# Kernel optimization log

Measured on AMD Instinct MI355X. Metric: run time of the kernel, lower is better.

Reference implementation:

```python
import jax, jax.numpy as jnp
import numpy as np


def conv2d_same(x, w, b=None):
    # x: [B,C,H,W], w: [O,I,kh,kw], stride 1, SAME padding (pad=1 for 3x3)
    out = jax.lax.conv_general_dilated(
        x, w, window_strides=(1, 1), padding='SAME',
        dimension_numbers=('NCHW', 'OIHW', 'NCHW'))
    if b is not None:
        out = out + b[None, :, None, None]
    return out


def deform_conv(x, offset, wd, k=3, pad=1, dg=4):
    # DCNv1: per-location offset-guided bilinear sampling + weighted accumulation.
    # x: [B,C,H,W]; offset: [B, dg*k*k*2, H, W] as (dy,dx) pairs per kernel tap;
    # wd: [O, C, k, k] (bias-free, as in mmcv DeformConv).
    B, C, H, W = x.shape
    cg = C // dg          # channels per deformable group
    K = k * k
    off = offset.reshape(B, dg, K, 2, H, W)
    dy, dx = off[:, :, :, 0], off[:, :, :, 1]          # [B,dg,K,H,W]
    ky = (jnp.arange(K) // k - pad).astype(x.dtype)    # kernel row offsets
    kx = (jnp.arange(K) % k - pad).astype(x.dtype)     # kernel col offsets
    hh = jnp.arange(H, dtype=x.dtype)
    ww = jnp.arange(W, dtype=x.dtype)
    py = dy + ky[None, None, :, None, None] + hh[None, None, None, :, None]
    px = dx + kx[None, None, :, None, None] + ww[None, None, None, None, :]
    y0 = jnp.floor(py); x0 = jnp.floor(px)
    wy1 = py - y0; wy0 = 1.0 - wy1
    wx1 = px - x0; wx0 = 1.0 - wx1
    xg = x.reshape(B, dg, cg, H * W)

    def gather(yi, xi):
        # zero outside the feature map (implicit zero padding of bilinear kernel)
        valid = (yi >= 0) & (yi < H) & (xi >= 0) & (xi < W)
        yc = jnp.clip(yi, 0, H - 1).astype(jnp.int32)
        xc = jnp.clip(xi, 0, W - 1).astype(jnp.int32)
        idx = (yc * W + xc).reshape(B, dg, 1, K * H * W)
        g = jnp.take_along_axis(xg, jnp.broadcast_to(idx, (B, dg, cg, K * H * W)), axis=-1)
        g = g.reshape(B, dg, cg, K, H, W)
        return g * valid[:, :, None].astype(x.dtype)

    val = (gather(y0, x0) * (wy0 * wx0)[:, :, None]
           + gather(y0, x0 + 1) * (wy0 * wx1)[:, :, None]
           + gather(y0 + 1, x0) * (wy1 * wx0)[:, :, None]
           + gather(y0 + 1, x0 + 1) * (wy1 * wx1)[:, :, None])  # [B,dg,cg,K,H,W]
    wr = wd.reshape(wd.shape[0], dg, cg, K)
    return jnp.einsum('ogck,bgckhw->bohw', wr, val)


def setup_inputs() -> dict:
    key = jax.random.key(0)
    k1, k2, k3, k4 = jax.random.split(key, 4)
    B, C, H, W = 8, 256, 64, 64
    dg, ks = 4, 3
    x = jax.random.normal(k1, (B, C, H, W), dtype=jnp.float32)
    w1 = jax.random.normal(k2, (C, C, 3, 3), dtype=jnp.float32) * 0.01
    b1 = jnp.zeros((C,), dtype=jnp.float32)
    w2 = jax.random.normal(k3, (dg * ks * ks * 2, C, 3, 3), dtype=jnp.float32) * 0.01
    b2 = jnp.zeros((dg * ks * ks * 2,), dtype=jnp.float32)
    wd = jax.random.normal(k4, (C, C, ks, ks), dtype=jnp.float32) * 0.01
    return {'x': x, 'w1': w1, 'b1': b1, 'w2': w2, 'b2': b2, 'wd': wd}


def reference(x, w1, b1, w2, b2, wd):
    # offset branch uses x.detach() in the original
    xd = jax.lax.stop_gradient(x)
    offset = conv2d_same(conv2d_same(xd, w1, b1), w2, b2)
    return jax.nn.relu(deform_conv(x, offset, wd, k=3, pad=1, dg=4))
```

## Files before the change

kernel.cpp:

```cpp
#include <hip/hip_runtime.h>
#include <hip/hip_bf16.h>


typedef __attribute__((ext_vector_type(8))) short bf16x8;
typedef __attribute__((ext_vector_type(4))) float f32x4;

static __device__ __forceinline__ ushort f2bf(float f) {
  __hip_bfloat16 h = __float2bfloat16(f);
  return *reinterpret_cast<ushort*>(&h);
}
static __device__ __forceinline__ float bf2f(ushort u) {
  union { uint u32; float f; } cv;
  cv.u32 = ((uint)u) << 16;
  return cv.f;
}

__global__ __launch_bounds__(256) void prep_weights(
    const float* __restrict__ w1, const float* __restrict__ w2,
    const float* __restrict__ wd,
    ushort* __restrict__ wt1s, ushort* __restrict__ wt2s,
    ushort* __restrict__ wtds) {
  const int N1 = 36 * 256 * 64;
  const int N2 = 36 * 80 * 64;
  const int N3 = 36 * 256 * 64;
  int total = N1 + N2 + N3;
  for (int i = blockIdx.x * 256 + threadIdx.x; i < total; i += gridDim.x * 256) {
    if (i < N1) {
      int e = i & 7, p = (i >> 3) & 7, co = (i >> 6) & 255, ti = i >> 14;
      int cc = ((p ^ (co & 7)) << 3) + e;
      int kk = ti >> 2, chunk = ti & 3;
      wt1s[i] = f2bf(w1[(co * 256 + chunk * 64 + cc) * 9 + kk]);
    } else if (i < N1 + N2) {
      int d = i - N1;
      int e = d & 7, p = (d >> 3) & 7;
      int r = d >> 6;
      int co = r % 80, ti = r / 80;
      int cc = ((p ^ (co & 7)) << 3) + e;
      int kk = ti >> 2, chunk = ti & 3;
      wt2s[d] = (co < 72) ? f2bf(w2[(co * 256 + chunk * 64 + cc) * 9 + kk])
                          : (ushort)0;
    } else {
      int d = i - N1 - N2;
      int e = d & 7, p = (d >> 3) & 7, co = (d >> 6) & 255, ti = d >> 14;
      int c = ((p ^ (co & 7)) << 3) + e;
      int g = ti / 9, kk = ti - g * 9;
      wtds[d] = f2bf(wd[(co * 256 + g * 64 + c) * 9 + kk]);
    }
  }
}

__global__ __launch_bounds__(256) void transpose_x(
    const float* __restrict__ x, ushort* __restrict__ xt) {
  int id = blockIdx.x;
  int y = id & 63, bg = id >> 6;
  int c = threadIdx.x & 63, xi = threadIdx.x >> 6;
  const float* ip = x + (((size_t)bg) << 18) + ((size_t)c << 12) + y * 64;
  ushort* op = xt + (((size_t)bg) << 18) + (size_t)y * 4096 + c;
#pragma unroll
  for (int j = 0; j < 16; ++j) {
    int xx = xi * 16 + j;
    op[(size_t)xx * 64] = f2bf(ip[xx]);
  }
}

template <int MODE, int MFR, int NFR, bool RELU, bool HASBIAS, bool OUT_CHLAST>
__global__ __launch_bounds__(128, 1) void fa_mfma4(
    const ushort* __restrict__ inT,
    const float* __restrict__ off,
    const char* __restrict__ wBs,
    const float* __restrict__ bias,
    void* __restrict__ outp,
    int co_total, int co_write) {
  constexpr int CO_TILE = NFR * 16;
  constexpr int TILE_B = CO_TILE * 128;
  constexpr int NCALLS = TILE_B / (128 * 16);
  constexpr int NRN = (MODE == 1) ? 8 : 2;
  __shared__ __align__(16) ushort Blds[2][CO_TILE * 64];

  int id = blockIdx.x;
  int id2 = (id & 7) * 64 + (id >> 3);
  int b = id2 >> 6, h = id2 & 63;
  int t = threadIdx.x;
  int wv = t >> 6, lane = t & 63;
  int ml = lane & 15, kc = lane >> 4;
  int ml7 = ml & 7;

  auto stage = [&](int ti, int bufsel) {
    const char* src0 = wBs + (size_t)ti * TILE_B + t * 16;
    ushort* dst0 = &Blds[bufsel][t * 8];
#pragma unroll
    for (int m = 0; m < NCALLS; ++m) {
      __builtin_amdgcn_global_load_lds(
          (const __attribute__((address_space(1))) void*)(src0 + m * 2048),
          (__attribute__((address_space(3))) void*)(dst0 + m * 1024), 16, 0, 0);
    }
  };

  int pcol[MFR];
#pragma unroll
  for (int mf = 0; mf < MFR; ++mf) pcol[mf] = wv * (MFR * 16) + mf * 16 + ml;

  const bf16x8 bz = {0, 0, 0, 0, 0, 0, 0, 0};
  bf16x8 aCur[MFR][2];
  bf16x8 rN[MFR][NRN];
  float wsv[MFR][4];
  float2 offA[MFR];

  auto issueA0 = [&](int tn) {
    int kk = tn >> 2, chunk = tn & 3;
    int ky = kk / 3, kx = kk - ky * 3;
    int gy = h + ky - 1;
    bool rowok = (gy >= 0) & (gy < 64);
#pragma unroll
    for (int mf = 0; mf < MFR; ++mf) {
      int gx = pcol[mf] + kx - 1;
      bool inb = rowok & (gx >= 0) & (gx < 64);
      const ushort* p =
          inT + ((((size_t)(b * 4 + chunk) << 12) + gy * 64 + gx) << 6) + kc * 8;
      rN[mf][0] = bz;
      rN[mf][1] = bz;
      if (inb) {
        rN[mf][0] = *(const bf16x8*)p;
        rN[mf][1] = *(const bf16x8*)(p + 32);
      }
    }
  };
  auto finishA0 = [&]() {
#pragma unroll
    for (int mf = 0; mf < MFR; ++mf) {
      aCur[mf][0] = rN[mf][0];
      aCur[mf][1] = rN[mf][1];
    }
  };

  auto loadOff = [&](int tn) {
    int g = tn / 9, kk = tn - 9 * (tn / 9);
    int ch = g * 18 + kk * 2;
#pragma unroll
    for (int mf = 0; mf < MFR; ++mf) {
      const float* offp =
          off + (((size_t)b * 72 + ch) << 12) + h * 64 + pcol[mf];
      offA[mf].x = offp[0];
      offA[mf].y = offp[4096];
    }
  };
  auto issueA1 = [&](int tn) {
    int g = tn / 9, kk = tn - 9 * (tn / 9);
    int ky = kk / 3, kx = kk - ky * 3;
    const ushort* base = inT + (((size_t)(b * 4 + g)) << 18) + kc * 8;
#pragma unroll
    for (int mf = 0; mf < MFR; ++mf) {
      float py = (float)(h + ky - 1) + offA[mf].x;
      float pxf = (float)(pcol[mf] + kx - 1) + offA[mf].y;
      float y0f = floorf(py), x0f = floorf(pxf);
      float wy1 = py - y0f, wx1 = pxf - x0f;
      float wy0 = 1.f - wy1, wx0 = 1.f - wx1;
      int y0 = (int)y0f, x0i = (int)x0f;
      int y1 = y0 + 1, x1i = x0i + 1;
      bool vy0 = (y0 >= 0) & (y0 < 64);
      bool vy1 = (y1 >= 0) & (y1 < 64);
      bool vx0 = (x0i >= 0) & (x0i < 64);
      bool vx1 = (x1i >= 0) & (x1i < 64);
      wsv[mf][0] = (vy0 & vx0) ? wy0 * wx0 : 0.f;
      wsv[mf][1] = (vy0 & vx1) ? wy0 * wx1 : 0.f;
      wsv[mf][2] = (vy1 & vx0) ? wy1 * wx0 : 0.f;
      wsv[mf][3] = (vy1 & vx1) ? wy1 * wx1 : 0.f;
      int yc0 = min(max(y0, 0), 63), yc1 = min(max(y1, 0), 63);
      int xc0 = min(max(x0i, 0), 63), xc1 = min(max(x1i, 0), 63);
      const ushort* p00 = base + ((yc0 * 64 + xc0) << 6);
      const ushort* p01 = base + ((yc0 * 64 + xc1) << 6);
      const ushort* p10 = base + ((yc1 * 64 + xc0) << 6);
      const ushort* p11 = base + ((yc1 * 64 + xc1) << 6);
      rN[mf][0] = *(const bf16x8*)p00;
      rN[mf][1] = *(const bf16x8*)(p00 + 32);
      rN[mf][2] = *(const bf16x8*)p01;
      rN[mf][3] = *(const bf16x8*)(p01 + 32);
      rN[mf][4] = *(const bf16x8*)p10;
      rN[mf][5] = *(const bf16x8*)(p10 + 32);
      rN[mf][6] = *(const bf16x8*)p11;
      rN[mf][7] = *(const bf16x8*)(p11 + 32);
    }
  };
  auto finishA1 = [&]() {
#pragma unroll
    for (int mf = 0; mf < MFR; ++mf) {
      float w00 = wsv[mf][0], w01 = wsv[mf][1];
      float w10 = wsv[mf][2], w11 = wsv[mf][3];
#pragma unroll
      for (int ks = 0; ks < 2; ++ks) {
        bf16x8 q00 = rN[mf][0 + ks], q01 = rN[mf][2 + ks];
        bf16x8 q10 = rN[mf][4 + ks], q11 = rN[mf][6 + ks];
        bf16x8 av;
#pragma unroll
        for (int jj = 0; jj < 4; ++jj) {
          float v0 = w00 * bf2f((ushort)q00[2 * jj]) + w01 * bf2f((ushort)q01[2 * jj]) +
                     w10 * bf2f((ushort)q10[2 * jj]) + w11 * bf2f((ushort)q11[2 * jj]);
          float v1 = w00 * bf2f((ushort)q00[2 * jj + 1]) + w01 * bf2f((ushort)q01[2 * jj + 1]) +
                     w10 * bf2f((ushort)q10[2 * jj + 1]) + w11 * bf2f((ushort)q11[2 * jj + 1]);
          av[2 * jj] = (short)f2bf(v0);
          av[2 * jj + 1] = (short)f2bf(v1);
        }
        aCur[mf][ks] = av;
      }
    }
  };

  f32x4 acc[MFR][NFR];
#pragma unroll
  for (int i = 0; i < MFR; ++i)
#pragma unroll
    for (int j = 0; j < NFR; ++j) acc[i][j] = (f32x4){0.f, 0.f, 0.f, 0.f};

  if (MODE == 1) {
    loadOff(0);
    issueA1(0);
    loadOff(1);
    finishA1();
  } else {
    issueA0(0);
    finishA0();
  }
  stage(0, 0);
  __syncthreads();

  for (int ti = 0; ti < 36; ++ti) {
    int cur = ti & 1;
    if (ti < 35) {
      stage(ti + 1, cur ^ 1);
      if (MODE == 1) issueA1(ti + 1); else issueA0(ti + 1);
    }
    if (MODE == 1 && ti < 34) loadOff(ti + 2);

#pragma unroll
    for (int ks = 0; ks < 2; ++ks) {
      int sw = (((ks * 4 + kc) ^ ml7) << 3);
      bf16x8 bq[NFR];
#pragma unroll
      for (int nf = 0; nf < NFR; ++nf)
        bq[nf] = *(const bf16x8*)&Blds[cur][(nf * 16 + ml) * 64 + sw];
#pragma unroll
      for (int mf = 0; mf < MFR; ++mf)
#pragma unroll
        for (int nf = 0; nf < NFR; ++nf)
          acc[mf][nf] = __builtin_amdgcn_mfma_f32_16x16x32_bf16(
              aCur[mf][ks], bq[nf], acc[mf][nf], 0, 0, 0);
    }

    if (ti < 35) { if (MODE == 1) finishA1(); else finishA0(); }
    __syncthreads();
  }

  int rq = lane >> 4;
#pragma unroll
  for (int nf = 0; nf < NFR; ++nf) {
    int cog = nf * 16 + ml;
    if (cog < co_write) {
      float bv = HASBIAS ? bias[cog] : 0.f;
#pragma unroll
      for (int mf = 0; mf < MFR; ++mf) {
#pragma unroll
        for (int ri = 0; ri < 4; ++ri) {
          int pxe = wv * (MFR * 16) + mf * 16 + rq * 4 + ri;
          float v = acc[mf][nf][ri] + bv;
          if (RELU) v = fmaxf(v, 0.f);
          if (OUT_CHLAST) {
            int g_out = cog >> 6, ci = cog & 63;
            ((ushort*)outp)[((((size_t)(b * 4 + g_out) << 12) + h * 64 + pxe) << 6) + ci] =
                f2bf(v);
          } else {
            ((float*)outp)[(((size_t)b * co_total + cog) << 12) + h * 64 + pxe] = v;
          }
        }
      }
    }
  }
}

extern "C" void kernel_launch(void* const* d_in, const int* in_sizes, int n_in,
                              void* d_out, int out_size, void* d_ws, size_t ws_size,
                              hipStream_t stream) {
  const float* x  = (const float*)d_in[0];
  const float* w1 = (const float*)d_in[1];
  const float* b1 = (const float*)d_in[2];
  const float* w2 = (const float*)d_in[3];
  const float* b2 = (const float*)d_in[4];
  const float* wd = (const float*)d_in[5];

  char* wsb = (char*)d_ws;
  float*  off_buf = (float*)wsb;
  ushort* xt      = (ushort*)(wsb + 9437184);
  ushort* wt1s    = (ushort*)(wsb + 26214400);
  ushort* wt2s    = (ushort*)(wsb + 27394048);
  ushort* wtds    = (ushort*)(wsb + 27762688);

  prep_weights<<<2048, 256, 0, stream>>>(w1, w2, wd, wt1s, wt2s, wtds);
  transpose_x<<<2048, 256, 0, stream>>>(x, xt);

  fa_mfma4<0, 2, 16, false, true, true>
      <<<512, 128, 0, stream>>>(xt, nullptr, (const char*)wt1s, b1, d_out, 256, 256);

  fa_mfma4<0, 2, 5, false, true, false>
      <<<512, 128, 0, stream>>>((const ushort*)d_out, nullptr, (const char*)wt2s,
                                b2, off_buf, 72, 72);

  fa_mfma4<1, 2, 16, true, false, false>
      <<<512, 128, 0, stream>>>(xt, off_buf, (const char*)wtds, nullptr, d_out,
                                256, 256);
}
```

Before: 204.3 us.

## Load weight fragments directly from global memory instead of LDS staging

Removes the double-buffered LDS staging of weight tiles (global_load_lds plus per-iteration __syncthreads) and has each lane read its B fragments straight from global memory, relying on L2/L1 caching. The weight prep no longer applies the XOR swizzle, since the swizzle was only there to avoid LDS bank conflicts. This drops the barriers and LDS traffic, at the cost of more per-wave global load latency and redundant reads of the same weights by both waves.

```diff
diff --git a/kernel.cpp b/kernel.cpp
--- a/kernel.cpp
+++ b/kernel.cpp
@@ -18,33 +18,29 @@
 __global__ __launch_bounds__(256) void prep_weights(
     const float* __restrict__ w1, const float* __restrict__ w2,
     const float* __restrict__ wd,
-    ushort* __restrict__ wt1s, ushort* __restrict__ wt2s,
-    ushort* __restrict__ wtds) {
+    ushort* __restrict__ wt1t, ushort* __restrict__ wt2t,
+    ushort* __restrict__ wtdt) {
   const int N1 = 36 * 256 * 64;
   const int N2 = 36 * 80 * 64;
   const int N3 = 36 * 256 * 64;
   int total = N1 + N2 + N3;
   for (int i = blockIdx.x * 256 + threadIdx.x; i < total; i += gridDim.x * 256) {
     if (i < N1) {
-      int e = i & 7, p = (i >> 3) & 7, co = (i >> 6) & 255, ti = i >> 14;
-      int cc = ((p ^ (co & 7)) << 3) + e;
+      int k6 = i & 63, co = (i >> 6) & 255, ti = i >> 14;
       int kk = ti >> 2, chunk = ti & 3;
-      wt1s[i] = f2bf(w1[(co * 256 + chunk * 64 + cc) * 9 + kk]);
+      wt1t[i] = f2bf(w1[(co * 256 + chunk * 64 + k6) * 9 + kk]);
     } else if (i < N1 + N2) {
       int d = i - N1;
-      int e = d & 7, p = (d >> 3) & 7;
-      int r = d >> 6;
+      int k6 = d & 63, r = d >> 6;
       int co = r % 80, ti = r / 80;
-      int cc = ((p ^ (co & 7)) << 3) + e;
       int kk = ti >> 2, chunk = ti & 3;
-      wt2s[d] = (co < 72) ? f2bf(w2[(co * 256 + chunk * 64 + cc) * 9 + kk])
+      wt2t[d] = (co < 72) ? f2bf(w2[(co * 256 + chunk * 64 + k6) * 9 + kk])
                           : (ushort)0;
     } else {
       int d = i - N1 - N2;
-      int e = d & 7, p = (d >> 3) & 7, co = (d >> 6) & 255, ti = d >> 14;
-      int c = ((p ^ (co & 7)) << 3) + e;
+      int k6 = d & 63, co = (d >> 6) & 255, ti = d >> 14;
       int g = ti / 9, kk = ti - g * 9;
-      wtds[d] = f2bf(wd[(co * 256 + g * 64 + c) * 9 + kk]);
+      wtdt[d] = f2bf(wd[(co * 256 + g * 64 + k6) * 9 + kk]);
     }
   }
 }
@@ -63,19 +59,17 @@
   }
 }
 
-template <int MODE, int MFR, int NFR, bool RELU, bool HASBIAS, bool OUT_CHLAST>
-__global__ __launch_bounds__(128, 1) void fa_mfma4(
+template <int MODE, int NFR, bool RELU, bool HASBIAS, bool OUT_CHLAST>
+__global__ __launch_bounds__(128, 1) void fa_mfma5(
     const ushort* __restrict__ inT,
     const float* __restrict__ off,
-    const char* __restrict__ wBs,
+    const ushort* __restrict__ wB,
     const float* __restrict__ bias,
     void* __restrict__ outp,
     int co_total, int co_write) {
+  constexpr int MFR = 2;
   constexpr int CO_TILE = NFR * 16;
-  constexpr int TILE_B = CO_TILE * 128;
-  constexpr int NCALLS = TILE_B / (128 * 16);
   constexpr int NRN = (MODE == 1) ? 8 : 2;
-  __shared__ __align__(16) ushort Blds[2][CO_TILE * 64];
 
   int id = blockIdx.x;
   int id2 = (id & 7) * 64 + (id >> 3);
@@ -83,18 +77,6 @@
   int t = threadIdx.x;
   int wv = t >> 6, lane = t & 63;
   int ml = lane & 15, kc = lane >> 4;
-  int ml7 = ml & 7;
-
-  auto stage = [&](int ti, int bufsel) {
-    const char* src0 = wBs + (size_t)ti * TILE_B + t * 16;
-    ushort* dst0 = &Blds[bufsel][t * 8];
-#pragma unroll
-    for (int m = 0; m < NCALLS; ++m) {
-      __builtin_amdgcn_global_load_lds(
-          (const __attribute__((address_space(1))) void*)(src0 + m * 2048),
-          (__attribute__((address_space(3))) void*)(dst0 + m * 1024), 16, 0, 0);
-    }
-  };
 
   int pcol[MFR];
 #pragma unroll
@@ -105,6 +87,8 @@
   bf16x8 rN[MFR][NRN];
   float wsv[MFR][4];
   float2 offA[MFR];
+
+  const ushort* wBl = wB + (ml << 6) + kc * 8;
 
   auto issueA0 = [&](int tn) {
     int kk = tn >> 2, chunk = tn & 3;
@@ -220,34 +204,41 @@
     issueA0(0);
     finishA0();
   }
-  stage(0, 0);
-  __syncthreads();
 
   for (int ti = 0; ti < 36; ++ti) {
-    int cur = ti & 1;
     if (ti < 35) {
-      stage(ti + 1, cur ^ 1);
       if (MODE == 1) issueA1(ti + 1); else issueA0(ti + 1);
     }
     if (MODE == 1 && ti < 34) loadOff(ti + 2);
 
-#pragma unroll
-    for (int ks = 0; ks < 2; ++ks) {
-      int sw = (((ks * 4 + kc) ^ ml7) << 3);
+    const ushort* wt = wBl + ((size_t)ti * CO_TILE << 6);
+
+    {
       bf16x8 bq[NFR];
 #pragma unroll
       for (int nf = 0; nf < NFR; ++nf)
-        bq[nf] = *(const bf16x8*)&Blds[cur][(nf * 16 + ml) * 64 + sw];
+        bq[nf] = *(const bf16x8*)(wt + (nf << 10));
 #pragma unroll
       for (int mf = 0; mf < MFR; ++mf)
 #pragma unroll
         for (int nf = 0; nf < NFR; ++nf)
           acc[mf][nf] = __builtin_amdgcn_mfma_f32_16x16x32_bf16(
-              aCur[mf][ks], bq[nf], acc[mf][nf], 0, 0, 0);
+              aCur[mf][0], bq[nf], acc[mf][nf], 0, 0, 0);
+    }
+    {
+      bf16x8 bq[NFR];
+#pragma unroll
+      for (int nf = 0; nf < NFR; ++nf)
+        bq[nf] = *(const bf16x8*)(wt + (nf << 10) + 32);
+#pragma unroll
+      for (int mf = 0; mf < MFR; ++mf)
+#pragma unroll
+        for (int nf = 0; nf < NFR; ++nf)
+          acc[mf][nf] = __builtin_amdgcn_mfma_f32_16x16x32_bf16(
+              aCur[mf][1], bq[nf], acc[mf][nf], 0, 0, 0);
     }
 
     if (ti < 35) { if (MODE == 1) finishA1(); else finishA0(); }
-    __syncthreads();
   }
 
   int rq = lane >> 4;
@@ -289,21 +280,20 @@
   char* wsb = (char*)d_ws;
   float*  off_buf = (float*)wsb;
   ushort* xt      = (ushort*)(wsb + 9437184);
-  ushort* wt1s    = (ushort*)(wsb + 26214400);
-  ushort* wt2s    = (ushort*)(wsb + 27394048);
-  ushort* wtds    = (ushort*)(wsb + 27762688);
-
-  prep_weights<<<2048, 256, 0, stream>>>(w1, w2, wd, wt1s, wt2s, wtds);
+  ushort* wt1t    = (ushort*)(wsb + 26214400);
+  ushort* wt2t    = (ushort*)(wsb + 27394048);
+  ushort* wtdt    = (ushort*)(wsb + 27762688);
+
+  prep_weights<<<2048, 256, 0, stream>>>(w1, w2, wd, wt1t, wt2t, wtdt);
   transpose_x<<<2048, 256, 0, stream>>>(x, xt);
 
-  fa_mfma4<0, 2, 16, false, true, true>
-      <<<512, 128, 0, stream>>>(xt, nullptr, (const char*)wt1s, b1, d_out, 256, 256);
-
-  fa_mfma4<0, 2, 5, false, true, false>
-      <<<512, 128, 0, stream>>>((const ushort*)d_out, nullptr, (const char*)wt2s,
-                                b2, off_buf, 72, 72);
-
-  fa_mfma4<1, 2, 16, true, false, false>
-      <<<512, 128, 0, stream>>>(xt, off_buf, (const char*)wtds, nullptr, d_out,
-                                256, 256);
-}
+  fa_mfma5<0, 16, false, true, true>
+      <<<512, 128, 0, stream>>>(xt, nullptr, wt1t, b1, d_out, 256, 256);
+
+  fa_mfma5<0, 5, false, true, false>
+      <<<512, 128, 0, stream>>>((const ushort*)d_out, nullptr, wt2t, b2,
+                                off_buf, 72, 72);
+
+  fa_mfma5<1, 16, true, false, false>
+      <<<512, 128, 0, stream>>>(xt, off_buf, wtdt, nullptr, d_out, 256, 256);
+}
```

Result: slower. 416.8 us (+104.0%).

## Split each row tile across four waves with one M-fragment each

Applied to the files above, without the earlier changes.

The conv/deform-conv MFMA kernel now launches 256 threads (4 waves) per row-block instead of 128 (2 waves). Each wave handles 16 pixels with a single M fragment rather than 32 pixels with two. Launch bounds allow 2 blocks per CU, and the weight staging is rewritten so 256 threads cover the tile with clamped addresses. The intent is to cut per-thread registers and raise occupancy and latency hiding for the gather-heavy deformable path. The cost is that each B-fragment LDS read now feeds half as many MFMAs, and the clamped staging re-reads some bytes.

```diff
diff --git a/kernel.cpp b/kernel.cpp
--- a/kernel.cpp
+++ b/kernel.cpp
@@ -63,8 +63,8 @@
   }
 }
 
-template <int MODE, int MFR, int NFR, bool RELU, bool HASBIAS, bool OUT_CHLAST>
-__global__ __launch_bounds__(128, 1) void fa_mfma4(
+template <int MODE, int NFR, bool RELU, bool HASBIAS, bool OUT_CHLAST>
+__global__ __launch_bounds__(256, 2) void fa_mfma6(
     const ushort* __restrict__ inT,
     const float* __restrict__ off,
     const char* __restrict__ wBs,
@@ -73,9 +73,9 @@
     int co_total, int co_write) {
   constexpr int CO_TILE = NFR * 16;
   constexpr int TILE_B = CO_TILE * 128;
-  constexpr int NCALLS = TILE_B / (128 * 16);
+  constexpr int NCALLS = (TILE_B + 4095) / 4096;
   constexpr int NRN = (MODE == 1) ? 8 : 2;
-  __shared__ __align__(16) ushort Blds[2][CO_TILE * 64];
+  __shared__ __align__(16) ushort Blds[2][NCALLS * 2048];
 
   int id = blockIdx.x;
   int id2 = (id & 7) * 64 + (id >> 3);
@@ -86,130 +86,109 @@
   int ml7 = ml & 7;
 
   auto stage = [&](int ti, int bufsel) {
-    const char* src0 = wBs + (size_t)ti * TILE_B + t * 16;
-    ushort* dst0 = &Blds[bufsel][t * 8];
 #pragma unroll
     for (int m = 0; m < NCALLS; ++m) {
+      int d = (m * 256 + t) * 16;
+      int ds = (d > TILE_B - 16) ? (TILE_B - 16) : d;
+      const char* src = wBs + (size_t)ti * TILE_B + ds;
+      ushort* dst = &Blds[bufsel][(m * 256 + t) * 8];
       __builtin_amdgcn_global_load_lds(
-          (const __attribute__((address_space(1))) void*)(src0 + m * 2048),
-          (__attribute__((address_space(3))) void*)(dst0 + m * 1024), 16, 0, 0);
-    }
-  };
-
-  int pcol[MFR];
-#pragma unroll
-  for (int mf = 0; mf < MFR; ++mf) pcol[mf] = wv * (MFR * 16) + mf * 16 + ml;
+          (const __attribute__((address_space(1))) void*)src,
+          (__attribute__((address_space(3))) void*)dst, 16, 0, 0);
+    }
+  };
+
+  const int pcol = wv * 16 + ml;
 
   const bf16x8 bz = {0, 0, 0, 0, 0, 0, 0, 0};
-  bf16x8 aCur[MFR][2];
-  bf16x8 rN[MFR][NRN];
-  float wsv[MFR][4];
-  float2 offA[MFR];
+  bf16x8 aCur[2];
+  bf16x8 rN[NRN];
+  float wsv[4];
+  float2 offA;
 
   auto issueA0 = [&](int tn) {
     int kk = tn >> 2, chunk = tn & 3;
     int ky = kk / 3, kx = kk - ky * 3;
-    int gy = h + ky - 1;
-    bool rowok = (gy >= 0) & (gy < 64);
-#pragma unroll
-    for (int mf = 0; mf < MFR; ++mf) {
-      int gx = pcol[mf] + kx - 1;
-      bool inb = rowok & (gx >= 0) & (gx < 64);
-      const ushort* p =
-          inT + ((((size_t)(b * 4 + chunk) << 12) + gy * 64 + gx) << 6) + kc * 8;
-      rN[mf][0] = bz;
-      rN[mf][1] = bz;
-      if (inb) {
-        rN[mf][0] = *(const bf16x8*)p;
-        rN[mf][1] = *(const bf16x8*)(p + 32);
-      }
+    int gy = h + ky - 1, gx = pcol + kx - 1;
+    bool inb = (gy >= 0) & (gy < 64) & (gx >= 0) & (gx < 64);
+    const ushort* p =
+        inT + ((((size_t)(b * 4 + chunk) << 12) + gy * 64 + gx) << 6) + kc * 8;
+    rN[0] = bz;
+    rN[1] = bz;
+    if (inb) {
+      rN[0] = *(const bf16x8*)p;
+      rN[1] = *(const bf16x8*)(p + 32);
     }
   };
   auto finishA0 = [&]() {
-#pragma unroll
-    for (int mf = 0; mf < MFR; ++mf) {
-      aCur[mf][0] = rN[mf][0];
-      aCur[mf][1] = rN[mf][1];
-    }
+    aCur[0] = rN[0];
+    aCur[1] = rN[1];
   };
 
   auto loadOff = [&](int tn) {
     int g = tn / 9, kk = tn - 9 * (tn / 9);
     int ch = g * 18 + kk * 2;
-#pragma unroll
-    for (int mf = 0; mf < MFR; ++mf) {
-      const float* offp =
-          off + (((size_t)b * 72 + ch) << 12) + h * 64 + pcol[mf];
-      offA[mf].x = offp[0];
-      offA[mf].y = offp[4096];
-    }
+    const float* offp = off + (((size_t)b * 72 + ch) << 12) + h * 64 + pcol;
+    offA.x = offp[0];
+    offA.y = offp[4096];
   };
   auto issueA1 = [&](int tn) {
     int g = tn / 9, kk = tn - 9 * (tn / 9);
     int ky = kk / 3, kx = kk - ky * 3;
     const ushort* base = inT + (((size_t)(b * 4 + g)) << 18) + kc * 8;
-#pragma unroll
-    for (int mf = 0; mf < MFR; ++mf) {
-      float py = (float)(h + ky - 1) + offA[mf].x;
-      float pxf = (float)(pcol[mf] + kx - 1) + offA[mf].y;
-      float y0f = floorf(py), x0f = floorf(pxf);
-      float wy1 = py - y0f, wx1 = pxf - x0f;
-      float wy0 = 1.f - wy1, wx0 = 1.f - wx1;
-      int y0 = (int)y0f, x0i = (int)x0f;
-      int y1 = y0 + 1, x1i = x0i + 1;
-      bool vy0 = (y0 >= 0) & (y0 < 64);
-      bool vy1 = (y1 >= 0) & (y1 < 64);
-      bool vx0 = (x0i >= 0) & (x0i < 64);
-      bool vx1 = (x1i >= 0) & (x1i < 64);
-      wsv[mf][0] = (vy0 & vx0) ? wy0 * wx0 : 0.f;
-      wsv[mf][1] = (vy0 & vx1) ? wy0 * wx1 : 0.f;
-      wsv[mf][2] = (vy1 & vx0) ? wy1 * wx0 : 0.f;
-      wsv[mf][3] = (vy1 & vx1) ? wy1 * wx1 : 0.f;
-      int yc0 = min(max(y0, 0), 63), yc1 = min(max(y1, 0), 63);
-      int xc0 = min(max(x0i, 0), 63), xc1 = min(max(x1i, 0), 63);
-      const ushort* p00 = base + ((yc0 * 64 + xc0) << 6);
-      const ushort* p01 = base + ((yc0 * 64 + xc1) << 6);
-      const ushort* p10 = base + ((yc1 * 64 + xc0) << 6);
-      const ushort* p11 = base + ((yc1 * 64 + xc1) << 6);
-      rN[mf][0] = *(const bf16x8*)p00;
-      rN[mf][1] = *(const bf16x8*)(p00 + 32);
-      rN[mf][2] = *(const bf16x8*)p01;
-      rN[mf][3] = *(const bf16x8*)(p01 + 32);
-      rN[mf][4] = *(const bf16x8*)p10;
-      rN[mf][5] = *(const bf16x8*)(p10 + 32);
-      rN[mf][6] = *(const bf16x8*)p11;
-      rN[mf][7] = *(const bf16x8*)(p11 + 32);
-    }
+    float py = (float)(h + ky - 1) + offA.x;
+    float pxf = (float)(pcol + kx - 1) + offA.y;
+    float y0f = floorf(py), x0f = floorf(pxf);
+    float wy1 = py - y0f, wx1 = pxf - x0f;
+    float wy0 = 1.f - wy1, wx0 = 1.f - wx1;
+    int y0 = (int)y0f, x0i = (int)x0f;
+    int y1 = y0 + 1, x1i = x0i + 1;
+    bool vy0 = (y0 >= 0) & (y0 < 64);
+    bool vy1 = (y1 >= 0) & (y1 < 64);
+    bool vx0 = (x0i >= 0) & (x0i < 64);
+    bool vx1 = (x1i >= 0) & (x1i < 64);
+    wsv[0] = (vy0 & vx0) ? wy0 * wx0 : 0.f;
+    wsv[1] = (vy0 & vx1) ? wy0 * wx1 : 0.f;
+    wsv[2] = (vy1 & vx0) ? wy1 * wx0 : 0.f;
+    wsv[3] = (vy1 & vx1) ? wy1 * wx1 : 0.f;
+    int yc0 = min(max(y0, 0), 63), yc1 = min(max(y1, 0), 63);
+    int xc0 = min(max(x0i, 0), 63), xc1 = min(max(x1i, 0), 63);
+    const ushort* p00 = base + ((yc0 * 64 + xc0) << 6);
+    const ushort* p01 = base + ((yc0 * 64 + xc1) << 6);
+    const ushort* p10 = base + ((yc1 * 64 + xc0) << 6);
+    const ushort* p11 = base + ((yc1 * 64 + xc1) << 6);
+    rN[0] = *(const bf16x8*)p00;
+    rN[1] = *(const bf16x8*)(p00 + 32);
+    rN[2] = *(const bf16x8*)p01;
+    rN[3] = *(const bf16x8*)(p01 + 32);
+    rN[4] = *(const bf16x8*)p10;
+    rN[5] = *(const bf16x8*)(p10 + 32);
+    rN[6] = *(const bf16x8*)p11;
+    rN[7] = *(const bf16x8*)(p11 + 32);
   };
   auto finishA1 = [&]() {
-#pragma unroll
-    for (int mf = 0; mf < MFR; ++mf) {
-      float w00 = wsv[mf][0], w01 = wsv[mf][1];
-      float w10 = wsv[mf][2], w11 = wsv[mf][3];
-#pragma unroll
-      for (int ks = 0; ks < 2; ++ks) {
-        bf16x8 q00 = rN[mf][0 + ks], q01 = rN[mf][2 + ks];
-        bf16x8 q10 = rN[mf][4 + ks], q11 = rN[mf][6 + ks];
-        bf16x8 av;
-#pragma unroll
-        for (int jj = 0; jj < 4; ++jj) {
-          float v0 = w00 * bf2f((ushort)q00[2 * jj]) + w01 * bf2f((ushort)q01[2 * jj]) +
-                     w10 * bf2f((ushort)q10[2 * jj]) + w11 * bf2f((ushort)q11[2 * jj]);
-          float v1 = w00 * bf2f((ushort)q00[2 * jj + 1]) + w01 * bf2f((ushort)q01[2 * jj + 1]) +
-                     w10 * bf2f((ushort)q10[2 * jj + 1]) + w11 * bf2f((ushort)q11[2 * jj + 1]);
-          av[2 * jj] = (short)f2bf(v0);
-          av[2 * jj + 1] = (short)f2bf(v1);
-        }
-        aCur[mf][ks] = av;
+    float w00 = wsv[0], w01 = wsv[1], w10 = wsv[2], w11 = wsv[3];
+#pragma unroll
+    for (int ks = 0; ks < 2; ++ks) {
+      bf16x8 q00 = rN[0 + ks], q01 = rN[2 + ks];
+      bf16x8 q10 = rN[4 + ks], q11 = rN[6 + ks];
+      bf16x8 av;
+#pragma unroll
+      for (int jj = 0; jj < 4; ++jj) {
+        float v0 = w00 * bf2f((ushort)q00[2 * jj]) + w01 * bf2f((ushort)q01[2 * jj]) +
+                   w10 * bf2f((ushort)q10[2 * jj]) + w11 * bf2f((ushort)q11[2 * jj]);
+        float v1 = w00 * bf2f((ushort)q00[2 * jj + 1]) + w01 * bf2f((ushort)q01[2 * jj + 1]) +
+                   w10 * bf2f((ushort)q10[2 * jj + 1]) + w11 * bf2f((ushort)q11[2 * jj + 1]);
+        av[2 * jj] = (short)f2bf(v0);
+        av[2 * jj + 1] = (short)f2bf(v1);
       }
-    }
-  };
-
-  f32x4 acc[MFR][NFR];
-#pragma unroll
-  for (int i = 0; i < MFR; ++i)
-#pragma unroll
-    for (int j = 0; j < NFR; ++j) acc[i][j] = (f32x4){0.f, 0.f, 0.f, 0.f};
+      aCur[ks] = av;
+    }
+  };
+
+  f32x4 acc[NFR];
+#pragma unroll
+  for (int j = 0; j < NFR; ++j) acc[j] = (f32x4){0.f, 0.f, 0.f, 0.f};
 
   if (MODE == 1) {
     loadOff(0);
@@ -239,11 +218,9 @@
       for (int nf = 0; nf < NFR; ++nf)
         bq[nf] = *(const bf16x8*)&Blds[cur][(nf * 16 + ml) * 64 + sw];
 #pragma unroll
-      for (int mf = 0; mf < MFR; ++mf)
-#pragma unroll
-        for (int nf = 0; nf < NFR; ++nf)
-          acc[mf][nf] = __builtin_amdgcn_mfma_f32_16x16x32_bf16(
-              aCur[mf][ks], bq[nf], acc[mf][nf], 0, 0, 0);
+      for (int nf = 0; nf < NFR; ++nf)
+        acc[nf] = __builtin_amdgcn_mfma_f32_16x16x32_bf16(
+            aCur[ks], bq[nf], acc[nf], 0, 0, 0);
     }
 
     if (ti < 35) { if (MODE == 1) finishA1(); else finishA0(); }
@@ -257,19 +234,16 @@
     if (cog < co_write) {
       float bv = HASBIAS ? bias[cog] : 0.f;
 #pragma unroll
-      for (int mf = 0; mf < MFR; ++mf) {
-#pragma unroll
-        for (int ri = 0; ri < 4; ++ri) {
-          int pxe = wv * (MFR * 16) + mf * 16 + rq * 4 + ri;
-          float v = acc[mf][nf][ri] + bv;
-          if (RELU) v = fmaxf(v, 0.f);
-          if (OUT_CHLAST) {
-            int g_out = cog >> 6, ci = cog & 63;
-            ((ushort*)outp)[((((size_t)(b * 4 + g_out) << 12) + h * 64 + pxe) << 6) + ci] =
-                f2bf(v);
-          } else {
-            ((float*)outp)[(((size_t)b * co_total + cog) << 12) + h * 64 + pxe] = v;
-          }
+      for (int ri = 0; ri < 4; ++ri) {
+        int pxe = wv * 16 + rq * 4 + ri;
+        float v = acc[nf][ri] + bv;
+        if (RELU) v = fmaxf(v, 0.f);
+        if (OUT_CHLAST) {
+          int g_out = cog >> 6, ci = cog & 63;
+          ((ushort*)outp)[((((size_t)(b * 4 + g_out) << 12) + h * 64 + pxe) << 6) + ci] =
+              f2bf(v);
+        } else {
+          ((float*)outp)[(((size_t)b * co_total + cog) << 12) + h * 64 + pxe] = v;
         }
       }
     }
@@ -296,14 +270,14 @@
   prep_weights<<<2048, 256, 0, stream>>>(w1, w2, wd, wt1s, wt2s, wtds);
   transpose_x<<<2048, 256, 0, stream>>>(x, xt);
 
-  fa_mfma4<0, 2, 16, false, true, true>
-      <<<512, 128, 0, stream>>>(xt, nullptr, (const char*)wt1s, b1, d_out, 256, 256);
-
-  fa_mfma4<0, 2, 5, false, true, false>
-      <<<512, 128, 0, stream>>>((const ushort*)d_out, nullptr, (const char*)wt2s,
+  fa_mfma6<0, 16, false, true, true>
+      <<<512, 256, 0, stream>>>(xt, nullptr, (const char*)wt1s, b1, d_out, 256, 256);
+
+  fa_mfma6<0, 5, false, true, false>
+      <<<512, 256, 0, stream>>>((const ushort*)d_out, nullptr, (const char*)wt2s,
                                 b2, off_buf, 72, 72);
 
-  fa_mfma4<1, 2, 16, true, false, false>
-      <<<512, 128, 0, stream>>>(xt, off_buf, (const char*)wtds, nullptr, d_out,
+  fa_mfma6<1, 16, true, false, false>
+      <<<512, 256, 0, stream>>>(xt, off_buf, (const char*)wtds, nullptr, d_out,
                                 256, 256);
 }
```

New measurement: 189.1 us. 1.08x faster.

## Split K across two blocks with 32x32 MFMA tiles and add partial-sum reduce kernels

Applied to the files above, without the earlier changes.

Each of the three GEMM-style kernels now covers two output rows with 256 threads using 32x32x16 bf16 MFMA instructions. The 36 K-steps are split into two halves handled by separate blocks, which write bf16 partial sums to workspace. New reduce kernels add the two halves, apply bias or ReLU, and convert layout. Weight swizzle patterns change and the offset-conv padding grows to 96 channels. This raises parallelism and occupancy and reuses operands better per MFMA, at the cost of extra partial-buffer traffic, three more launches, and bf16 rounding of the partial sums.

```diff
diff --git a/kernel.cpp b/kernel.cpp
--- a/kernel.cpp
+++ b/kernel.cpp
@@ -3,7 +3,7 @@
 
 
 typedef __attribute__((ext_vector_type(8))) short bf16x8;
-typedef __attribute__((ext_vector_type(4))) float f32x4;
+typedef __attribute__((ext_vector_type(16))) float f32x16;
 
 static __device__ __forceinline__ ushort f2bf(float f) {
   __hip_bfloat16 h = __float2bfloat16(f);
@@ -13,6 +13,9 @@
   union { uint u32; float f; } cv;
   cv.u32 = ((uint)u) << 16;
   return cv.f;
+}
+static __device__ __forceinline__ int swq(int co) {
+  return ((co & 7) + ((co >> 3) & 3)) & 7;
 }
 
 __global__ __launch_bounds__(256) void prep_weights(
@@ -21,28 +24,28 @@
     ushort* __restrict__ wt1s, ushort* __restrict__ wt2s,
     ushort* __restrict__ wtds) {
   const int N1 = 36 * 256 * 64;
-  const int N2 = 36 * 80 * 64;
+  const int N2 = 36 * 96 * 64;
   const int N3 = 36 * 256 * 64;
   int total = N1 + N2 + N3;
   for (int i = blockIdx.x * 256 + threadIdx.x; i < total; i += gridDim.x * 256) {
     if (i < N1) {
       int e = i & 7, p = (i >> 3) & 7, co = (i >> 6) & 255, ti = i >> 14;
-      int cc = ((p ^ (co & 7)) << 3) + e;
+      int cc = ((p ^ swq(co)) << 3) + e;
       int kk = ti >> 2, chunk = ti & 3;
       wt1s[i] = f2bf(w1[(co * 256 + chunk * 64 + cc) * 9 + kk]);
     } else if (i < N1 + N2) {
       int d = i - N1;
       int e = d & 7, p = (d >> 3) & 7;
       int r = d >> 6;
-      int co = r % 80, ti = r / 80;
-      int cc = ((p ^ (co & 7)) << 3) + e;
+      int co = r % 96, ti = r / 96;
+      int cc = ((p ^ swq(co)) << 3) + e;
       int kk = ti >> 2, chunk = ti & 3;
       wt2s[d] = (co < 72) ? f2bf(w2[(co * 256 + chunk * 64 + cc) * 9 + kk])
                           : (ushort)0;
     } else {
       int d = i - N1 - N2;
       int e = d & 7, p = (d >> 3) & 7, co = (d >> 6) & 255, ti = d >> 14;
-      int c = ((p ^ (co & 7)) << 3) + e;
+      int c = ((p ^ swq(co)) << 3) + e;
       int g = ti / 9, kk = ti - g * 9;
       wtds[d] = f2bf(wd[(co * 256 + g * 64 + c) * 9 + kk]);
     }
@@ -63,95 +66,110 @@
   }
 }
 
-template <int MODE, int MFR, int NFR, bool RELU, bool HASBIAS, bool OUT_CHLAST>
-__global__ __launch_bounds__(128, 1) void fa_mfma4(
+template <int MODE, int NFR, bool CHLAST>
+__global__ __launch_bounds__(256, 2) void fa_mfma7(
     const ushort* __restrict__ inT,
     const float* __restrict__ off,
     const char* __restrict__ wBs,
-    const float* __restrict__ bias,
-    void* __restrict__ outp,
-    int co_total, int co_write) {
-  constexpr int CO_TILE = NFR * 16;
+    ushort* __restrict__ parA,
+    ushort* __restrict__ parB,
+    int co_write) {
+  constexpr int CO_TILE = NFR * 32;
   constexpr int TILE_B = CO_TILE * 128;
-  constexpr int NCALLS = TILE_B / (128 * 16);
-  constexpr int NRN = (MODE == 1) ? 8 : 2;
+  constexpr int NCALLS = TILE_B / 4096;
   __shared__ __align__(16) ushort Blds[2][CO_TILE * 64];
 
   int id = blockIdx.x;
   int id2 = (id & 7) * 64 + (id >> 3);
-  int b = id2 >> 6, h = id2 & 63;
+  int khalf = id2 & 1;
+  int rest = id2 >> 1;
+  int hp = rest & 31, b = rest >> 5;
+  int h0 = hp * 2;
   int t = threadIdx.x;
   int wv = t >> 6, lane = t & 63;
-  int ml = lane & 15, kc = lane >> 4;
-  int ml7 = ml & 7;
-
-  auto stage = [&](int ti, int bufsel) {
-    const char* src0 = wBs + (size_t)ti * TILE_B + t * 16;
+  int c31 = lane & 31, kc2 = lane >> 5;
+  int qr = swq(c31);
+  int pxl = wv * 32 + c31;
+  int row = h0 + (pxl >> 6), col = pxl & 63;
+  ushort* par = khalf ? parB : parA;
+
+  auto stage = [&](int tloc, int bufsel) {
+    const char* src0 = wBs + (size_t)(khalf * 18 + tloc) * TILE_B + t * 16;
     ushort* dst0 = &Blds[bufsel][t * 8];
 #pragma unroll
     for (int m = 0; m < NCALLS; ++m) {
       __builtin_amdgcn_global_load_lds(
-          (const __attribute__((address_space(1))) void*)(src0 + m * 2048),
-          (__attribute__((address_space(3))) void*)(dst0 + m * 1024), 16, 0, 0);
+          (const __attribute__((address_space(1))) void*)(src0 + m * 4096),
+          (__attribute__((address_space(3))) void*)(dst0 + m * 2048), 16, 0, 0);
     }
   };
 
-  int pcol[MFR];
-#pragma unroll
-  for (int mf = 0; mf < MFR; ++mf) pcol[mf] = wv * (MFR * 16) + mf * 16 + ml;
+  f32x16 acc[NFR];
+#pragma unroll
+  for (int j = 0; j < NFR; ++j)
+#pragma unroll
+    for (int r = 0; r < 16; ++r) acc[j][r] = 0.f;
 
   const bf16x8 bz = {0, 0, 0, 0, 0, 0, 0, 0};
-  bf16x8 aCur[MFR][2];
-  bf16x8 rN[MFR][NRN];
-  float wsv[MFR][4];
-  float2 offA[MFR];
-
-  auto issueA0 = [&](int tn) {
-    int kk = tn >> 2, chunk = tn & 3;
-    int ky = kk / 3, kx = kk - ky * 3;
-    int gy = h + ky - 1;
-    bool rowok = (gy >= 0) & (gy < 64);
-#pragma unroll
-    for (int mf = 0; mf < MFR; ++mf) {
-      int gx = pcol[mf] + kx - 1;
-      bool inb = rowok & (gx >= 0) & (gx < 64);
+
+  if (MODE == 0) {
+    bf16x8 rN[4];
+    auto issueA0 = [&](int tg) {
+      int kk = tg >> 2, ch = tg & 3;
+      int ky = kk / 3, kx = kk - ky * 3;
+      int gy = row + ky - 1, gx = col + kx - 1;
+      bool inb = (gy >= 0) & (gy < 64) & (gx >= 0) & (gx < 64);
       const ushort* p =
-          inT + ((((size_t)(b * 4 + chunk) << 12) + gy * 64 + gx) << 6) + kc * 8;
-      rN[mf][0] = bz;
-      rN[mf][1] = bz;
-      if (inb) {
-        rN[mf][0] = *(const bf16x8*)p;
-        rN[mf][1] = *(const bf16x8*)(p + 32);
-      }
-    }
-  };
-  auto finishA0 = [&]() {
-#pragma unroll
-    for (int mf = 0; mf < MFR; ++mf) {
-      aCur[mf][0] = rN[mf][0];
-      aCur[mf][1] = rN[mf][1];
-    }
-  };
-
-  auto loadOff = [&](int tn) {
-    int g = tn / 9, kk = tn - 9 * (tn / 9);
-    int ch = g * 18 + kk * 2;
-#pragma unroll
-    for (int mf = 0; mf < MFR; ++mf) {
+          inT + ((((size_t)(b * 4 + ch) << 12) + gy * 64 + gx) << 6) + kc2 * 8;
+#pragma unroll
+      for (int ks = 0; ks < 4; ++ks)
+        rN[ks] = inb ? *(const bf16x8*)(p + ks * 16) : bz;
+    };
+
+    issueA0(khalf * 18);
+    stage(0, 0);
+    __syncthreads();
+
+    for (int tloc = 0; tloc < 18; ++tloc) {
+      int cur = tloc & 1;
+      bf16x8 aC[4];
+#pragma unroll
+      for (int ks = 0; ks < 4; ++ks) aC[ks] = rN[ks];
+      if (tloc < 17) {
+        stage(tloc + 1, cur ^ 1);
+        issueA0(khalf * 18 + tloc + 1);
+      }
+#pragma unroll
+      for (int ks = 0; ks < 4; ++ks) {
+        int slot = ((2 * ks + kc2) ^ qr) << 3;
+#pragma unroll
+        for (int nf = 0; nf < NFR; ++nf) {
+          bf16x8 bq = *(const bf16x8*)&Blds[cur][(nf * 32 + c31) * 64 + slot];
+          acc[nf] = __builtin_amdgcn_mfma_f32_32x32x16_bf16(aC[ks], bq, acc[nf], 0, 0, 0);
+        }
+      }
+      if (tloc < 17) __syncthreads();
+    }
+  } else {
+    uint oC[4];
+    float wC[4];
+    const ushort* plC;
+    float2 offN;
+    bf16x8 rN[8];
+
+    auto loadOff = [&](int tg) {
+      int g = tg / 9, kk = tg - 9 * (tg / 9);
       const float* offp =
-          off + (((size_t)b * 72 + ch) << 12) + h * 64 + pcol[mf];
-      offA[mf].x = offp[0];
-      offA[mf].y = offp[4096];
-    }
-  };
-  auto issueA1 = [&](int tn) {
-    int g = tn / 9, kk = tn - 9 * (tn / 9);
-    int ky = kk / 3, kx = kk - ky * 3;
-    const ushort* base = inT + (((size_t)(b * 4 + g)) << 18) + kc * 8;
-#pragma unroll
-    for (int mf = 0; mf < MFR; ++mf) {
-      float py = (float)(h + ky - 1) + offA[mf].x;
-      float pxf = (float)(pcol[mf] + kx - 1) + offA[mf].y;
+          off + (((size_t)b * 72 + g * 18 + kk * 2) << 12) + row * 64 + col;
+      offN.x = offp[0];
+      offN.y = offp[4096];
+    };
+    auto calcAddr = [&](int tg, float2 oa, uint* o4, float* w4,
+                        const ushort*& pl) {
+      int g = tg / 9, kk = tg - 9 * (tg / 9);
+      int ky = kk / 3, kx = kk - ky * 3;
+      float py = (float)(row + ky - 1) + oa.x;
+      float pxf = (float)(col + kx - 1) + oa.y;
       float y0f = floorf(py), x0f = floorf(pxf);
       float wy1 = py - y0f, wx1 = pxf - x0f;
       float wy0 = 1.f - wy1, wx0 = 1.f - wx1;
@@ -161,118 +179,179 @@
       bool vy1 = (y1 >= 0) & (y1 < 64);
       bool vx0 = (x0i >= 0) & (x0i < 64);
       bool vx1 = (x1i >= 0) & (x1i < 64);
-      wsv[mf][0] = (vy0 & vx0) ? wy0 * wx0 : 0.f;
-      wsv[mf][1] = (vy0 & vx1) ? wy0 * wx1 : 0.f;
-      wsv[mf][2] = (vy1 & vx0) ? wy1 * wx0 : 0.f;
-      wsv[mf][3] = (vy1 & vx1) ? wy1 * wx1 : 0.f;
+      w4[0] = (vy0 & vx0) ? wy0 * wx0 : 0.f;
+      w4[1] = (vy0 & vx1) ? wy0 * wx1 : 0.f;
+      w4[2] = (vy1 & vx0) ? wy1 * wx0 : 0.f;
+      w4[3] = (vy1 & vx1) ? wy1 * wx1 : 0.f;
       int yc0 = min(max(y0, 0), 63), yc1 = min(max(y1, 0), 63);
       int xc0 = min(max(x0i, 0), 63), xc1 = min(max(x1i, 0), 63);
-      const ushort* p00 = base + ((yc0 * 64 + xc0) << 6);
-      const ushort* p01 = base + ((yc0 * 64 + xc1) << 6);
-      const ushort* p10 = base + ((yc1 * 64 + xc0) << 6);
-      const ushort* p11 = base + ((yc1 * 64 + xc1) << 6);
-      rN[mf][0] = *(const bf16x8*)p00;
-      rN[mf][1] = *(const bf16x8*)(p00 + 32);
-      rN[mf][2] = *(const bf16x8*)p01;
-      rN[mf][3] = *(const bf16x8*)(p01 + 32);
-      rN[mf][4] = *(const bf16x8*)p10;
-      rN[mf][5] = *(const bf16x8*)(p10 + 32);
-      rN[mf][6] = *(const bf16x8*)p11;
-      rN[mf][7] = *(const bf16x8*)(p11 + 32);
-    }
-  };
-  auto finishA1 = [&]() {
-#pragma unroll
-    for (int mf = 0; mf < MFR; ++mf) {
-      float w00 = wsv[mf][0], w01 = wsv[mf][1];
-      float w10 = wsv[mf][2], w11 = wsv[mf][3];
+      o4[0] = (uint)((yc0 * 64 + xc0) << 6);
+      o4[1] = (uint)((yc0 * 64 + xc1) << 6);
+      o4[2] = (uint)((yc1 * 64 + xc0) << 6);
+      o4[3] = (uint)((yc1 * 64 + xc1) << 6);
+      pl = inT + (((size_t)(b * 4 + g)) << 18) + kc2 * 8;
+    };
+    auto gather = [&](const ushort* pl, const uint* o4, int hs) {
+#pragma unroll
+      for (int cr = 0; cr < 4; ++cr) {
+        rN[cr * 2] = *(const bf16x8*)(pl + o4[cr] + (hs * 2) * 16);
+        rN[cr * 2 + 1] = *(const bf16x8*)(pl + o4[cr] + (hs * 2 + 1) * 16);
+      }
+    };
+    auto finish = [&](const float* w4, bf16x8& a0, bf16x8& a1) {
+#pragma unroll
+      for (int ksl = 0; ksl < 2; ++ksl) {
+        bf16x8 q0 = rN[0 + ksl], q1 = rN[2 + ksl], q2 = rN[4 + ksl], q3 = rN[6 + ksl];
+        bf16x8 av;
+#pragma unroll
+        for (int e = 0; e < 8; ++e) {
+          float v = w4[0] * bf2f((ushort)q0[e]) + w4[1] * bf2f((ushort)q1[e]) +
+                    w4[2] * bf2f((ushort)q2[e]) + w4[3] * bf2f((ushort)q3[e]);
+          av[e] = (short)f2bf(v);
+        }
+        if (ksl == 0) a0 = av; else a1 = av;
+      }
+    };
+
+    loadOff(khalf * 18);
+    calcAddr(khalf * 18, offN, oC, wC, plC);
+    gather(plC, oC, 0);
+    loadOff(khalf * 18 + 1);
+    stage(0, 0);
+    __syncthreads();
+
+    for (int tloc = 0; tloc < 18; ++tloc) {
+      int tg = khalf * 18 + tloc;
+      int cur = tloc & 1;
+      if (tloc < 17) stage(tloc + 1, cur ^ 1);
+
+      bf16x8 a0, a1;
+      finish(wC, a0, a1);
+      gather(plC, oC, 1);
 #pragma unroll
       for (int ks = 0; ks < 2; ++ks) {
-        bf16x8 q00 = rN[mf][0 + ks], q01 = rN[mf][2 + ks];
-        bf16x8 q10 = rN[mf][4 + ks], q11 = rN[mf][6 + ks];
-        bf16x8 av;
-#pragma unroll
-        for (int jj = 0; jj < 4; ++jj) {
-          float v0 = w00 * bf2f((ushort)q00[2 * jj]) + w01 * bf2f((ushort)q01[2 * jj]) +
-                     w10 * bf2f((ushort)q10[2 * jj]) + w11 * bf2f((ushort)q11[2 * jj]);
-          float v1 = w00 * bf2f((ushort)q00[2 * jj + 1]) + w01 * bf2f((ushort)q01[2 * jj + 1]) +
-                     w10 * bf2f((ushort)q10[2 * jj + 1]) + w11 * bf2f((ushort)q11[2 * jj + 1]);
-          av[2 * jj] = (short)f2bf(v0);
-          av[2 * jj + 1] = (short)f2bf(v1);
-        }
-        aCur[mf][ks] = av;
-      }
-    }
-  };
-
-  f32x4 acc[MFR][NFR];
-#pragma unroll
-  for (int i = 0; i < MFR; ++i)
-#pragma unroll
-    for (int j = 0; j < NFR; ++j) acc[i][j] = (f32x4){0.f, 0.f, 0.f, 0.f};
-
-  if (MODE == 1) {
-    loadOff(0);
-    issueA1(0);
-    loadOff(1);
-    finishA1();
-  } else {
-    issueA0(0);
-    finishA0();
-  }
-  stage(0, 0);
+        int slot = ((2 * ks + kc2) ^ qr) << 3;
+        bf16x8 a = ks ? a1 : a0;
+#pragma unroll
+        for (int nf = 0; nf < NFR; ++nf) {
+          bf16x8 bq = *(const bf16x8*)&Blds[cur][(nf * 32 + c31) * 64 + slot];
+          acc[nf] = __builtin_amdgcn_mfma_f32_32x32x16_bf16(a, bq, acc[nf], 0, 0, 0);
+        }
+      }
+
+      uint oN[4];
+      float wN[4];
+      const ushort* plN = plC;
+      if (tloc < 17) calcAddr(tg + 1, offN, oN, wN, plN);
+      if (tloc < 16) loadOff(tg + 2);
+
+      finish(wC, a0, a1);
+      if (tloc < 17) gather(plN, oN, 0);
+#pragma unroll
+      for (int ks = 2; ks < 4; ++ks) {
+        int slot = ((2 * ks + kc2) ^ qr) << 3;
+        bf16x8 a = (ks == 2) ? a0 : a1;
+#pragma unroll
+        for (int nf = 0; nf < NFR; ++nf) {
+          bf16x8 bq = *(const bf16x8*)&Blds[cur][(nf * 32 + c31) * 64 + slot];
+          acc[nf] = __builtin_amdgcn_mfma_f32_32x32x16_bf16(a, bq, acc[nf], 0, 0, 0);
+        }
+      }
+
+      if (tloc < 17) {
+#pragma unroll
+        for (int cr = 0; cr < 4; ++cr) { oC[cr] = oN[cr]; wC[cr] = wN[cr]; }
+        plC = plN;
+        __syncthreads();
+      }
+    }
+  }
+
+#pragma unroll
+  for (int nf = 0; nf < NFR; ++nf) {
+    int cog = nf * 32 + c31;
+    if (cog < co_write) {
+#pragma unroll
+      for (int r = 0; r < 16; ++r) {
+        int pxb = wv * 32 + (r & 3) + 8 * (r >> 2) + 4 * kc2;
+        ushort v = f2bf(acc[nf][r]);
+        if (CHLAST) {
+          par[((((size_t)(b * 4 + (cog >> 6)) << 12) + h0 * 64 + pxb) << 6) +
+              (cog & 63)] = v;
+        } else {
+          par[(((size_t)b * co_write + cog) << 12) + h0 * 64 + pxb] = v;
+        }
+      }
+    }
+  }
+}
+
+__global__ __launch_bounds__(256) void reduce_c1(
+    const ushort* __restrict__ p0, const ushort* __restrict__ p1,
+    const float* __restrict__ bias, ushort* __restrict__ t1) {
+  const int N8 = (8 * 4 * 4096 * 64) / 8;
+  for (int i = blockIdx.x * 256 + threadIdx.x; i < N8; i += gridDim.x * 256) {
+    size_t base = (size_t)i * 8;
+    bf16x8 a = *(const bf16x8*)(p0 + base);
+    bf16x8 c = *(const bf16x8*)(p1 + base);
+    int c0 = (int)(base & 63);
+    int g = (int)((base >> 18) & 3);
+    bf16x8 o;
+#pragma unroll
+    for (int j = 0; j < 8; ++j) {
+      float v = bf2f((ushort)a[j]) + bf2f((ushort)c[j]) + bias[g * 64 + c0 + j];
+      o[j] = (short)f2bf(v);
+    }
+    *(bf16x8*)(t1 + base) = o;
+  }
+}
+
+__global__ __launch_bounds__(256) void reduce_c2(
+    const ushort* __restrict__ p0, const ushort* __restrict__ p1,
+    const float* __restrict__ bias, float* __restrict__ out) {
+  const int N8 = (8 * 72 * 4096) / 8;
+  for (int i = blockIdx.x * 256 + threadIdx.x; i < N8; i += gridDim.x * 256) {
+    size_t base = (size_t)i * 8;
+    bf16x8 a = *(const bf16x8*)(p0 + base);
+    bf16x8 c = *(const bf16x8*)(p1 + base);
+    int co = (int)((base >> 12) % 72);
+    float bv = bias[co];
+    float4 o0, o1;
+    o0.x = bf2f((ushort)a[0]) + bf2f((ushort)c[0]) + bv;
+    o0.y = bf2f((ushort)a[1]) + bf2f((ushort)c[1]) + bv;
+    o0.z = bf2f((ushort)a[2]) + bf2f((ushort)c[2]) + bv;
+    o0.w = bf2f((ushort)a[3]) + bf2f((ushort)c[3]) + bv;
+    o1.x = bf2f((ushort)a[4]) + bf2f((ushort)c[4]) + bv;
+    o1.y = bf2f((ushort)a[5]) + bf2f((ushort)c[5]) + bv;
+    o1.z = bf2f((ushort)a[6]) + bf2f((ushort)c[6]) + bv;
+    o1.w = bf2f((ushort)a[7]) + bf2f((ushort)c[7]) + bv;
+    *(float4*)(out + base) = o0;
+    *(float4*)(out + base + 4) = o1;
+  }
+}
+
+__global__ __launch_bounds__(256) void reduce_df(
+    const ushort* __restrict__ p0, const ushort* __restrict__ p1,
+    float* __restrict__ out) {
+  __shared__ float ts[64][65];
+  int bid = blockIdx.x;
+  int pt = bid & 63, cq = (bid >> 6) & 3, b = bid >> 8;
+  int t = threadIdx.x;
+  int c = t & 63, ty = t >> 6;
+  size_t inbase = (((size_t)(b * 4 + cq) << 12) + pt * 64) << 6;
+#pragma unroll 4
+  for (int s = 0; s < 16; ++s) {
+    int pxi = ty * 16 + s;
+    size_t idx = inbase + ((size_t)pxi << 6) + c;
+    float v = bf2f(p0[idx]) + bf2f(p1[idx]);
+    ts[c][pxi] = fmaxf(v, 0.f);
+  }
   __syncthreads();
-
-  for (int ti = 0; ti < 36; ++ti) {
-    int cur = ti & 1;
-    if (ti < 35) {
-      stage(ti + 1, cur ^ 1);
-      if (MODE == 1) issueA1(ti + 1); else issueA0(ti + 1);
-    }
-    if (MODE == 1 && ti < 34) loadOff(ti + 2);
-
-#pragma unroll
-    for (int ks = 0; ks < 2; ++ks) {
-      int sw = (((ks * 4 + kc) ^ ml7) << 3);
-      bf16x8 bq[NFR];
-#pragma unroll
-      for (int nf = 0; nf < NFR; ++nf)
-        bq[nf] = *(const bf16x8*)&Blds[cur][(nf * 16 + ml) * 64 + sw];
-#pragma unroll
-      for (int mf = 0; mf < MFR; ++mf)
-#pragma unroll
-        for (int nf = 0; nf < NFR; ++nf)
-          acc[mf][nf] = __builtin_amdgcn_mfma_f32_16x16x32_bf16(
-              aCur[mf][ks], bq[nf], acc[mf][nf], 0, 0, 0);
-    }
-
-    if (ti < 35) { if (MODE == 1) finishA1(); else finishA0(); }
-    __syncthreads();
-  }
-
-  int rq = lane >> 4;
-#pragma unroll
-  for (int nf = 0; nf < NFR; ++nf) {
-    int cog = nf * 16 + ml;
-    if (cog < co_write) {
-      float bv = HASBIAS ? bias[cog] : 0.f;
-#pragma unroll
-      for (int mf = 0; mf < MFR; ++mf) {
-#pragma unroll
-        for (int ri = 0; ri < 4; ++ri) {
-          int pxe = wv * (MFR * 16) + mf * 16 + rq * 4 + ri;
-          float v = acc[mf][nf][ri] + bv;
-          if (RELU) v = fmaxf(v, 0.f);
-          if (OUT_CHLAST) {
-            int g_out = cog >> 6, ci = cog & 63;
-            ((ushort*)outp)[((((size_t)(b * 4 + g_out) << 12) + h * 64 + pxe) << 6) + ci] =
-                f2bf(v);
-          } else {
-            ((float*)outp)[(((size_t)b * co_total + cog) << 12) + h * 64 + pxe] = v;
-          }
-        }
-      }
-    }
+  int px = t & 63;
+#pragma unroll 4
+  for (int s = 0; s < 16; ++s) {
+    int coi = ty * 16 + s;
+    out[(((size_t)b * 256 + cq * 64 + coi) << 12) + pt * 64 + px] = ts[coi][px];
   }
 }
 
@@ -291,19 +370,24 @@
   ushort* xt      = (ushort*)(wsb + 9437184);
   ushort* wt1s    = (ushort*)(wsb + 26214400);
   ushort* wt2s    = (ushort*)(wsb + 27394048);
-  ushort* wtds    = (ushort*)(wsb + 27762688);
+  ushort* wtds    = (ushort*)(wsb + 27836416);
+  ushort* par0    = (ushort*)(wsb + 29016064);
+  ushort* par1    = (ushort*)(wsb + 45793280);
 
   prep_weights<<<2048, 256, 0, stream>>>(w1, w2, wd, wt1s, wt2s, wtds);
   transpose_x<<<2048, 256, 0, stream>>>(x, xt);
 
-  fa_mfma4<0, 2, 16, false, true, true>
-      <<<512, 128, 0, stream>>>(xt, nullptr, (const char*)wt1s, b1, d_out, 256, 256);
-
-  fa_mfma4<0, 2, 5, false, true, false>
-      <<<512, 128, 0, stream>>>((const ushort*)d_out, nullptr, (const char*)wt2s,
-                                b2, off_buf, 72, 72);
-
-  fa_mfma4<1, 2, 16, true, false, false>
-      <<<512, 128, 0, stream>>>(xt, off_buf, (const char*)wtds, nullptr, d_out,
-                                256, 256);
-}
+  ushort* t1 = (ushort*)d_out;
+
+  fa_mfma7<0, 8, true><<<512, 256, 0, stream>>>(
+      xt, nullptr, (const char*)wt1s, par0, par1, 256);
+  reduce_c1<<<2048, 256, 0, stream>>>(par0, par1, b1, t1);
+
+  fa_mfma7<0, 3, false><<<512, 256, 0, stream>>>(
+      t1, nullptr, (const char*)wt2s, par0, par1, 72);
+  reduce_c2<<<1024, 256, 0, stream>>>(par0, par1, b2, off_buf);
+
+  fa_mfma7<1, 8, true><<<512, 256, 0, stream>>>(
+      xt, off_buf, (const char*)wtds, par0, par1, 256);
+  reduce_df<<<2048, 256, 0, stream>>>(par0, par1, (float*)d_out);
+}
```

Measured after the change: 197.0 us. 1.04x faster.
